# Performance work log

Hardware: AMD Instinct MI355X
Metric: run time of the kernel (lower is better)

## Reference

```python
import jax, jax.numpy as jnp
import numpy as np

B, S, D, P, R, NL = 16, 2048, 1024, 8192, 16, 64  # docs, seq, d_model, pairs, n_relations, n_label_pairs
MAX_SPAN = 32


def setup_inputs() -> dict:
    key = jax.random.key(0)
    ks = jax.random.split(key, 8)
    tokvecs = jax.random.normal(ks[0], (B, S, D), dtype=jnp.float32)
    batch_idx = jax.random.randint(ks[1], (P,), 0, B, dtype=jnp.int32)
    e1s = jax.random.randint(ks[2], (P,), 0, S - MAX_SPAN, dtype=jnp.int32)
    e1e = e1s + 1 + jax.random.randint(ks[3], (P,), 0, MAX_SPAN - 1, dtype=jnp.int32)
    e2s = jax.random.randint(ks[4], (P,), 0, S - MAX_SPAN, dtype=jnp.int32)
    e2e = e2s + 1 + jax.random.randint(ks[5], (P,), 0, MAX_SPAN - 1, dtype=jnp.int32)
    rel_idx = jax.random.randint(ks[6], (P,), 0, NL, dtype=jnp.int32)
    # multi-hot relationship-inclusion table (0/1 entries, as built in __init__)
    rel_table = (jax.random.uniform(ks[7], (NL, R)) < 0.25).astype(jnp.float32)
    return {
        "tokvecs": tokvecs,
        "batch_idx": batch_idx,
        "ent1_start": e1s,
        "ent1_end": e1e,
        "ent2_start": e2s,
        "ent2_end": e2e,
        "rel_idx": rel_idx,
        "rel_table": rel_table,
    }


def _span_mean(cs, b, s, e):
    # cs: [B, S+1, D] exclusive prefix sums; span mean = (cs[e] - cs[s]) / (e - s)
    seg = cs[b, e] - cs[b, s]                      # [P, D]
    return seg / (e - s)[:, None].astype(seg.dtype)


def reference(tokvecs, batch_idx, ent1_start, ent1_end, ent2_start, ent2_end, rel_idx, rel_table):
    Bn, Sn, Dn = tokvecs.shape
    # exclusive prefix sum along sequence -> O(1) mean per span instead of ragged gathers
    cs = jnp.concatenate(
        [jnp.zeros((Bn, 1, Dn), tokvecs.dtype), jnp.cumsum(tokvecs, axis=1)], axis=1
    )                                               # [B, S+1, D]
    m1 = _span_mean(cs, batch_idx, ent1_start, ent1_end)   # [P, D]
    m2 = _span_mean(cs, batch_idx, ent2_start, ent2_end)   # [P, D]
    rel = rel_table[rel_idx]                                # [P, R]
    return jnp.concatenate([m1, m2, rel], axis=-1)          # [P, 2D + R]
```

## Files before the change

kernel.cpp:

```cpp
#include <hip/hip_runtime.h>

#define S_LEN      2048
#define D_DIM      1024
#define R_DIM      16
#define OUT_STRIDE 2064
#define NBUCK      8192
#define BPT        8
#define GROUP      4
#define NR         4

__global__ __launch_bounds__(1024) void sort_jobs(
    const int* __restrict__ bidx, const int* __restrict__ e1s,
    const int* __restrict__ e2s, int* __restrict__ sorted, int njobs)
{
    __shared__ int hist[NBUCK];
    __shared__ int part[1024];
    const int t = threadIdx.x;

#pragma unroll
    for (int i = 0; i < BPT; ++i) hist[t * BPT + i] = 0;
    __syncthreads();

    for (int j = t; j < njobs; j += 1024) {
        const int p = j >> 1;
        const int s = (j & 1) ? e2s[p] : e1s[p];
        atomicAdd(&hist[(bidx[p] * S_LEN + s) >> 2], 1);
    }
    __syncthreads();

    int v[BPT];
    int sum = 0;
#pragma unroll
    for (int i = 0; i < BPT; ++i) { v[i] = hist[t * BPT + i]; sum += v[i]; }
    part[t] = sum;
    __syncthreads();
    for (int off = 1; off < 1024; off <<= 1) {
        int x = (t >= off) ? part[t - off] : 0;
        __syncthreads();
        part[t] += x;
        __syncthreads();
    }
    int run = (t == 0) ? 0 : part[t - 1];
#pragma unroll
    for (int i = 0; i < BPT; ++i) { int c = v[i]; hist[t * BPT + i] = run; run += c; }
    __syncthreads();

    for (int j = t; j < njobs; j += 1024) {
        const int p = j >> 1;
        const int s = (j & 1) ? e2s[p] : e1s[p];
        const int pos = atomicAdd(&hist[(bidx[p] * S_LEN + s) >> 2], 1);
        sorted[pos] = j;
    }
}

__device__ __forceinline__ void load16_lds(const float* g, float* l) {
    __builtin_amdgcn_global_load_lds(
        (const __attribute__((address_space(1))) void*)g,
        (__attribute__((address_space(3))) void*)l, 16, 0, 0);
}

__global__ __launch_bounds__(256) void gather_lds(
    const float* __restrict__ tok,
    const int*   __restrict__ sorted,
    const int*   __restrict__ bidx,
    const int*   __restrict__ e1s, const int* __restrict__ e1e,
    const int*   __restrict__ e2s, const int* __restrict__ e2e,
    const int*   __restrict__ ridx,
    const float* __restrict__ rtab,
    float*       __restrict__ out)
{
    __shared__ float buf[2][NR * D_DIM];

    const int blk = blockIdx.x;
    const int g  = (blk & 7) * (gridDim.x >> 3) + (blk >> 3);
    const int t  = threadIdx.x;
    const int wv = t >> 6;
    const int ln = t & 63;

    int   jp[GROUP], jh[GROUP], js[GROUP], je[GROUP];
    float jw[GROUP];
    int mins = 0x7fffffff, maxe = 0;
#pragma unroll
    for (int i = 0; i < GROUP; ++i) {
        const int id = __builtin_amdgcn_readfirstlane(sorted[g * GROUP + i]);
        const int p  = id >> 1;
        const int h  = id & 1;
        const int b  = __builtin_amdgcn_readfirstlane(bidx[p]);
        const int s  = __builtin_amdgcn_readfirstlane(h ? e2s[p] : e1s[p]);
        const int e  = __builtin_amdgcn_readfirstlane(h ? e2e[p] : e1e[p]);
        jp[i] = p; jh[i] = h;
        js[i] = b * S_LEN + s;
        je[i] = b * S_LEN + e;
        jw[i] = 1.0f / (float)(e - s);
        mins  = min(mins, js[i]);
        maxe  = max(maxe, je[i]);
    }

    const int nrows = maxe - mins;
    const int rmaxg = maxe - 1;
    const int niter = (nrows + NR - 1) / NR;

    auto stage = [&](int bi, int c) {
        const int grow = min(mins + c * NR + wv, rmaxg);
        const float* src = tok + (size_t)grow * D_DIM + ln * 4;
        float* dst = &buf[bi][wv * D_DIM];
#pragma unroll
        for (int q = 0; q < 4; ++q)
            load16_lds(src + q * 256, dst + q * 256);
    };

    stage(0, 0);

    float4 acc[GROUP];
#pragma unroll
    for (int i = 0; i < GROUP; ++i) acc[i] = make_float4(0.f, 0.f, 0.f, 0.f);

    __syncthreads();

    for (int c = 0; c < niter; ++c) {
        if (c + 1 < niter) stage((c + 1) & 1, c + 1);

        const int cb  = c & 1;
        const int gr0 = mins + c * NR;
#pragma unroll
        for (int r = 0; r < NR; ++r) {
            const float4 v = *reinterpret_cast<const float4*>(
                &buf[cb][r * D_DIM + t * 4]);
            const int gr = gr0 + r;
#pragma unroll
            for (int i = 0; i < GROUP; ++i) {
                const float w = (gr >= js[i] && gr < je[i]) ? jw[i] : 0.f;
                acc[i].x += v.x * w;
                acc[i].y += v.y * w;
                acc[i].z += v.z * w;
                acc[i].w += v.w * w;
            }
        }
        __syncthreads();
    }

#pragma unroll
    for (int i = 0; i < GROUP; ++i) {
        float* dst = out + (size_t)jp[i] * OUT_STRIDE + jh[i] * D_DIM + t * 4;
        *reinterpret_cast<float4*>(dst) = acc[i];
        if (jh[i] == 0 && t < 4) {
            const float4 rv = *reinterpret_cast<const float4*>(
                rtab + ridx[jp[i]] * R_DIM + t * 4);
            *reinterpret_cast<float4*>(
                out + (size_t)jp[i] * OUT_STRIDE + 2 * D_DIM + t * 4) = rv;
        }
    }
}

extern "C" void kernel_launch(void* const* d_in, const int* in_sizes, int n_in,
                              void* d_out, int out_size, void* d_ws, size_t ws_size,
                              hipStream_t stream) {
    const float* tok  = (const float*)d_in[0];
    const int*   bidx = (const int*)d_in[1];
    const int*   e1s  = (const int*)d_in[2];
    const int*   e1e  = (const int*)d_in[3];
    const int*   e2s  = (const int*)d_in[4];
    const int*   e2e  = (const int*)d_in[5];
    const int*   ridx = (const int*)d_in[6];
    const float* rtab = (const float*)d_in[7];
    float*       out  = (float*)d_out;

    const int P     = in_sizes[1];
    const int njobs = 2 * P;

    int* sorted = (int*)d_ws;

    sort_jobs<<<1, 1024, 0, stream>>>(bidx, e1s, e2s, sorted, njobs);

    const int nblocks = njobs / GROUP;
    gather_lds<<<nblocks, 256, 0, stream>>>(
        tok, sorted, bidx, e1s, e1e, e2s, e2e, ridx, rtab, out);
}
```

Before: 268.2 us.

## Group 16 sorted span jobs per block and split the feature dimension in half

Each block now handles 16 sorted span jobs instead of 4, and the 1024-wide feature dimension is split across two blocks of 128 threads, each covering a 512-column half. Rows staged into LDS are shared by more overlapping spans, which cuts redundant row reads from global memory. The cost is more accumulator registers (16 float4 per thread), possibly lower occupancy, and a wider row range per group, so more rows are scanned per job when spans in a group are far apart.

```diff
diff --git a/kernel.cpp b/kernel.cpp
--- a/kernel.cpp
+++ b/kernel.cpp
@@ -6,8 +6,9 @@
 #define OUT_STRIDE 2064
 #define NBUCK      8192
 #define BPT        8
-#define GROUP      4
+#define G          16
 #define NR         4
+#define HW         512
 
 __global__ __launch_bounds__(1024) void sort_jobs(
     const int* __restrict__ bidx, const int* __restrict__ e1s,
@@ -53,13 +54,13 @@
     }
 }
 
-__device__ __forceinline__ void load16_lds(const float* g, float* l) {
+__device__ __forceinline__ void load16_lds(const float* g_, float* l_) {
     __builtin_amdgcn_global_load_lds(
-        (const __attribute__((address_space(1))) void*)g,
-        (__attribute__((address_space(3))) void*)l, 16, 0, 0);
+        (const __attribute__((address_space(1))) void*)g_,
+        (__attribute__((address_space(3))) void*)l_, 16, 0, 0);
 }
 
-__global__ __launch_bounds__(256) void gather_lds(
+__global__ __launch_bounds__(128) void gather_g16(
     const float* __restrict__ tok,
     const int*   __restrict__ sorted,
     const int*   __restrict__ bidx,
@@ -69,31 +70,34 @@
     const float* __restrict__ rtab,
     float*       __restrict__ out)
 {
-    __shared__ float buf[2][NR * D_DIM];
+    __shared__ float buf[2][NR * HW];
 
     const int blk = blockIdx.x;
-    const int g  = (blk & 7) * (gridDim.x >> 3) + (blk >> 3);
+    const int w  = (blk & 7) * (gridDim.x >> 3) + (blk >> 3);
+    const int g  = w >> 1;
+    const int ch = w & 1;
     const int t  = threadIdx.x;
     const int wv = t >> 6;
     const int ln = t & 63;
 
-    int   jp[GROUP], jh[GROUP], js[GROUP], je[GROUP];
-    float jw[GROUP];
+    int   js[G], je[G], jd[G], jrel[G];
+    float jw[G];
     int mins = 0x7fffffff, maxe = 0;
 #pragma unroll
-    for (int i = 0; i < GROUP; ++i) {
-        const int id = __builtin_amdgcn_readfirstlane(sorted[g * GROUP + i]);
+    for (int i = 0; i < G; ++i) {
+        const int id = __builtin_amdgcn_readfirstlane(sorted[g * G + i]);
         const int p  = id >> 1;
         const int h  = id & 1;
         const int b  = __builtin_amdgcn_readfirstlane(bidx[p]);
         const int s  = __builtin_amdgcn_readfirstlane(h ? e2s[p] : e1s[p]);
         const int e  = __builtin_amdgcn_readfirstlane(h ? e2e[p] : e1e[p]);
-        jp[i] = p; jh[i] = h;
-        js[i] = b * S_LEN + s;
-        je[i] = b * S_LEN + e;
-        jw[i] = 1.0f / (float)(e - s);
-        mins  = min(mins, js[i]);
-        maxe  = max(maxe, je[i]);
+        js[i]   = b * S_LEN + s;
+        je[i]   = b * S_LEN + e;
+        jw[i]   = 1.0f / (float)(e - s);
+        jd[i]   = p * OUT_STRIDE + h * D_DIM;
+        jrel[i] = (h == 0) ? p : -1;
+        mins = min(mins, js[i]);
+        maxe = max(maxe, je[i]);
     }
 
     const int nrows = maxe - mins;
@@ -101,19 +105,22 @@
     const int niter = (nrows + NR - 1) / NR;
 
     auto stage = [&](int bi, int c) {
-        const int grow = min(mins + c * NR + wv, rmaxg);
-        const float* src = tok + (size_t)grow * D_DIM + ln * 4;
-        float* dst = &buf[bi][wv * D_DIM];
 #pragma unroll
-        for (int q = 0; q < 4; ++q)
-            load16_lds(src + q * 256, dst + q * 256);
+        for (int rr = 0; rr < 2; ++rr) {
+            const int r    = wv * 2 + rr;
+            const int grow = min(mins + c * NR + r, rmaxg);
+            const float* src = tok + (size_t)grow * D_DIM + ch * HW + ln * 4;
+            float* dst = &buf[bi][r * HW];
+            load16_lds(src,       dst);
+            load16_lds(src + 256, dst + 256);
+        }
     };
 
     stage(0, 0);
 
-    float4 acc[GROUP];
+    float4 acc[G];
 #pragma unroll
-    for (int i = 0; i < GROUP; ++i) acc[i] = make_float4(0.f, 0.f, 0.f, 0.f);
+    for (int i = 0; i < G; ++i) acc[i] = make_float4(0.f, 0.f, 0.f, 0.f);
 
     __syncthreads();
 
@@ -125,29 +132,29 @@
 #pragma unroll
         for (int r = 0; r < NR; ++r) {
             const float4 v = *reinterpret_cast<const float4*>(
-                &buf[cb][r * D_DIM + t * 4]);
+                &buf[cb][r * HW + t * 4]);
             const int gr = gr0 + r;
 #pragma unroll
-            for (int i = 0; i < GROUP; ++i) {
-                const float w = (gr >= js[i] && gr < je[i]) ? jw[i] : 0.f;
-                acc[i].x += v.x * w;
-                acc[i].y += v.y * w;
-                acc[i].z += v.z * w;
-                acc[i].w += v.w * w;
+            for (int i = 0; i < G; ++i) {
+                const float wt = (gr >= js[i] && gr < je[i]) ? jw[i] : 0.f;
+                acc[i].x += v.x * wt;
+                acc[i].y += v.y * wt;
+                acc[i].z += v.z * wt;
+                acc[i].w += v.w * wt;
             }
         }
         __syncthreads();
     }
 
 #pragma unroll
-    for (int i = 0; i < GROUP; ++i) {
-        float* dst = out + (size_t)jp[i] * OUT_STRIDE + jh[i] * D_DIM + t * 4;
+    for (int i = 0; i < G; ++i) {
+        float* dst = out + (size_t)jd[i] + ch * HW + t * 4;
         *reinterpret_cast<float4*>(dst) = acc[i];
-        if (jh[i] == 0 && t < 4) {
+        if (ch == 0 && jrel[i] >= 0 && t < 4) {
             const float4 rv = *reinterpret_cast<const float4*>(
-                rtab + ridx[jp[i]] * R_DIM + t * 4);
+                rtab + ridx[jrel[i]] * R_DIM + t * 4);
             *reinterpret_cast<float4*>(
-                out + (size_t)jp[i] * OUT_STRIDE + 2 * D_DIM + t * 4) = rv;
+                out + (size_t)jrel[i] * OUT_STRIDE + 2 * D_DIM + t * 4) = rv;
         }
     }
 }
@@ -172,7 +179,7 @@
 
     sort_jobs<<<1, 1024, 0, stream>>>(bidx, e1s, e2s, sorted, njobs);
 
-    const int nblocks = njobs / GROUP;
-    gather_lds<<<nblocks, 256, 0, stream>>>(
+    const int nblocks = (njobs / G) * 2;
+    gather_g16<<<nblocks, 128, 0, stream>>>(
         tok, sorted, bidx, e1s, e1e, e2s, e2e, ridx, rtab, out);
 }
```

New measurement: 293.7 us. +9.5%, slower.
